# Performance work log

Measured on AMD Instinct MI355X. Metric: run time of the kernel, lower is better.

## Reference

```python
import jax, jax.numpy as jnp
import numpy as np

BINS = 10
LOSS_WEIGHT = 1.0
N = 8388608


def setup_inputs() -> dict:
    key = jax.random.key(0)
    k1, k2 = jax.random.split(key)
    pred = jax.random.normal(k1, (N, 2), dtype=jnp.float32)
    target = jax.random.randint(k2, (N,), 0, 2, dtype=jnp.int64)
    return {"pred": pred, "target": target}


def reference(pred, target):
    # one-hot binary target, as in torch scatter_(1, target, 1) with class_num=2
    tgt = jax.nn.one_hot(target, 2, dtype=pred.dtype)  # [N, 2]
    # label_weight defaults to ones -> all elements valid
    tot = jnp.maximum(jnp.asarray(pred.size, pred.dtype), 1.0)

    # gradient magnitude g = |sigmoid(pred).detach() - target|, in [0, 1]
    g = jnp.abs(jax.nn.sigmoid(jax.lax.stop_gradient(pred)) - tgt)

    # edges are i/bins with edges[-1] += 1e-6, so bin = min(floor(g*bins), bins-1)
    bin_idx = jnp.clip((g * BINS).astype(jnp.int32), 0, BINS - 1)  # [N, 2]

    # histogram of valid samples per bin (all valid here)
    counts = jax.ops.segment_sum(
        jnp.ones((pred.size,), pred.dtype), bin_idx.reshape(-1), num_segments=BINS
    )  # [BINS]

    n_nonempty = (counts > 0).sum()
    per_bin_w = jnp.where(counts > 0, tot / jnp.maximum(counts, 1.0), 0.0)  # [BINS]
    weights = per_bin_w[bin_idx]  # [N, 2]
    weights = jnp.where(
        n_nonempty > 0, weights / n_nonempty.astype(pred.dtype), weights
    )
    weights = jax.lax.stop_gradient(weights)

    # stable BCE with logits: max(x,0) - x*t + log(1 + exp(-|x|))
    bce = jnp.maximum(pred, 0.0) - pred * tgt + jnp.log1p(jnp.exp(-jnp.abs(pred)))
    loss = jnp.sum(weights * bce) / tot
    return loss * LOSS_WEIGHT
```

## Files before the change

### kernel.cpp

```cpp
#include <hip/hip_runtime.h>

#define BINS 10
#define BLOCK 256
#define GRID 2048
#define NCOPY 8
#define CSTRIDE 32

#define LOG2E 1.44269504088896340736f
#define LN2   0.6931471805599453094


__constant__ const float THR[9] = {
    -2.1972246f, -1.3862944f, -0.84729785f, -0.40546511f, 0.0f,
     0.40546511f, 0.84729785f, 1.3862944f,  2.1972246f };

__global__ void ghmc_init(double* ws) {
    int i = threadIdx.x;
    if (i < NCOPY * CSTRIDE) ws[i] = 0.0;
}

__device__ __forceinline__ void proc(float y, float* __restrict__ s,
                                     unsigned* __restrict__ c) {
    y = fminf(fmaxf(y, -80.0f), 80.0f);
    float u  = __builtin_amdgcn_exp2f(y * LOG2E);
    float d  = 1.0f + u;
    float lg = __builtin_amdgcn_logf(d);
    s[0] += lg;
#pragma unroll
    for (int k = 0; k < 9; ++k) {
        bool cond = y >= THR[k];
        c[k] += (unsigned)__popcll(__ballot(cond));
        s[k + 1] += cond ? lg : 0.0f;
    }
}

__device__ __forceinline__ void proc_row(float x0, float x1, int t,
                                         float* __restrict__ s,
                                         unsigned* __restrict__ c) {
    unsigned s0 = (unsigned)(t ^ 1) << 31;
    unsigned s1 = s0 ^ 0x80000000u;
    proc(__uint_as_float(__float_as_uint(x0) ^ s0), s, c);
    proc(__uint_as_float(__float_as_uint(x1) ^ s1), s, c);
}

__global__ __launch_bounds__(BLOCK, 8) void ghmc_main(
    const float4* __restrict__ pred4,
    const int4*   __restrict__ tgt4,
    double* __restrict__ wsd,
    int nQuads, int nRows)
{
    const int tid = threadIdx.x;
    float    s[BINS];
    unsigned c[9];
#pragma unroll
    for (int b = 0; b < BINS; ++b) s[b] = 0.0f;
#pragma unroll
    for (int k = 0; k < 9; ++k) c[k] = 0u;

    for (int i = blockIdx.x * BLOCK + tid; i < nQuads; i += GRID * BLOCK) {
        float4 pa = pred4[2 * i + 0];
        float4 pb = pred4[2 * i + 1];
        int4   tq = tgt4[i];
        proc_row(pa.x, pa.y, tq.x, s, c);
        proc_row(pa.z, pa.w, tq.y, s, c);
        proc_row(pb.x, pb.y, tq.z, s, c);
        proc_row(pb.z, pb.w, tq.w, s, c);
    }

    if (blockIdx.x == 0 && tid == 0) {
        const float* pf = (const float*)pred4;
        const int*   tf = (const int*)tgt4;
        for (int r = nQuads * 4; r < nRows; ++r)
            proc_row(pf[2 * r], pf[2 * r + 1], tf[r], s, c);
    }

#pragma unroll
    for (int off = 32; off > 0; off >>= 1) {
#pragma unroll
        for (int b = 0; b < BINS; ++b) s[b] += __shfl_down(s[b], off, 64);
    }

    __shared__ float    sred[4][BINS];
    __shared__ unsigned cred[4][9];
    const int wid  = tid >> 6;
    const int lane = tid & 63;
    if (lane == 0) {
#pragma unroll
        for (int b = 0; b < BINS; ++b) sred[wid][b] = s[b];
#pragma unroll
        for (int k = 0; k < 9; ++k) cred[wid][k] = c[k];
    }
    __syncthreads();

    double* wcopy = wsd + (blockIdx.x & (NCOPY - 1)) * CSTRIDE;
    if (tid < BINS) {
        float S = sred[0][tid] + sred[1][tid] + sred[2][tid] + sred[3][tid];
        atomicAdd(&wcopy[tid], (double)S);
    } else if (tid >= 16 && tid < 25) {
        int k = tid - 16;
        unsigned C = cred[0][k] + cred[1][k] + cred[2][k] + cred[3][k];
        atomicAdd(&wcopy[10 + k], (double)C);
    }
}

__global__ __launch_bounds__(64) void ghmc_fin(
    const double* __restrict__ wsd, float* __restrict__ out, int nRows)
{
    const int tid = threadIdx.x;
    __shared__ double vals[19];
    if (tid < 19) {
        double a = 0.0;
#pragma unroll
        for (int r = 0; r < NCOPY; ++r) a += wsd[r * CSTRIDE + tid];
        vals[tid] = a;
    }
    __syncthreads();
    if (tid == 0) {
        double C[BINS + 1], S[BINS + 1];
        C[0] = 2.0 * (double)nRows;
#pragma unroll
        for (int k = 1; k <= 9; ++k) C[k] = vals[9 + k];
        C[BINS] = 0.0;
#pragma unroll
        for (int b = 0; b < BINS; ++b) S[b] = vals[b];
        S[BINS] = 0.0;
        int nz = 0;
        double acc = 0.0;
#pragma unroll
        for (int b = 0; b < BINS; ++b) {
            double cnt = C[b] - C[b + 1];
            double sm  = (S[b] - S[b + 1]) * LN2;
            if (cnt > 0.0) { nz++; acc += sm / cnt; }
        }
        out[0] = (float)((nz > 0) ? (acc / (double)nz) : 0.0);
    }
}

extern "C" void kernel_launch(void* const* d_in, const int* in_sizes, int n_in,
                              void* d_out, int out_size, void* d_ws, size_t ws_size,
                              hipStream_t stream) {
    const float* pred = (const float*)d_in[0];
    const int* target = (const int*)d_in[1];
    const int nRows = in_sizes[1];
    const int nQuads = nRows / 4;
    double* wsd = (double*)d_ws;
    float* out = (float*)d_out;

    ghmc_init<<<1, 256, 0, stream>>>(wsd);
    ghmc_main<<<GRID, BLOCK, 0, stream>>>(
        (const float4*)pred, (const int4*)target, wsd, nQuads, nRows);
    ghmc_fin<<<1, 64, 0, stream>>>(wsd, out, nRows);
}
```

Before: 33.34 us.

## Replace threshold ballot scan with per-thread LDS histogram of bin counts and sums

Each element now gets its bin index directly from the sigmoid value and increments a private per-thread float2 (count, log-sum) slot in shared memory. This replaces the nine threshold compares, ballots, popcounts and conditional adds per element. The loop is also restructured so each wave reads contiguous float4/int2 chunks, and the block reduction runs over the LDS histogram before the atomics. It adds a reciprocal and a read-modify-write to shared memory per element, and per-thread float counts could lose precision.

New measurement: 34.43 us. 1.03x slower.

```diff
diff --git a/kernel.cpp b/kernel.cpp
--- a/kernel.cpp
+++ b/kernel.cpp
@@ -10,105 +10,120 @@
 #define LN2   0.6931471805599453094
 
 
-__constant__ const float THR[9] = {
-    -2.1972246f, -1.3862944f, -0.84729785f, -0.40546511f, 0.0f,
-     0.40546511f, 0.84729785f, 1.3862944f,  2.1972246f };
-
 __global__ void ghmc_init(double* ws) {
     int i = threadIdx.x;
     if (i < NCOPY * CSTRIDE) ws[i] = 0.0;
 }
 
-__device__ __forceinline__ void proc(float y, float* __restrict__ s,
-                                     unsigned* __restrict__ c) {
+__device__ __forceinline__ void proc(float y, float2* __restrict__ hcol) {
     y = fminf(fmaxf(y, -80.0f), 80.0f);
     float u  = __builtin_amdgcn_exp2f(y * LOG2E);
     float d  = 1.0f + u;
+    float r  = __builtin_amdgcn_rcpf(d);
     float lg = __builtin_amdgcn_logf(d);
-    s[0] += lg;
-#pragma unroll
-    for (int k = 0; k < 9; ++k) {
-        bool cond = y >= THR[k];
-        c[k] += (unsigned)__popcll(__ballot(cond));
-        s[k + 1] += cond ? lg : 0.0f;
-    }
+    float sg = u * r;
+    int b = (int)(sg * 10.0f);
+    b = b > (BINS - 1) ? (BINS - 1) : b;
+    float2* h = hcol + (b << 8);
+    float2 v = *h;
+    v.x += 1.0f;
+    v.y += lg;
+    *h = v;
 }
 
 __device__ __forceinline__ void proc_row(float x0, float x1, int t,
-                                         float* __restrict__ s,
-                                         unsigned* __restrict__ c) {
+                                         float2* __restrict__ hcol) {
     unsigned s0 = (unsigned)(t ^ 1) << 31;
     unsigned s1 = s0 ^ 0x80000000u;
-    proc(__uint_as_float(__float_as_uint(x0) ^ s0), s, c);
-    proc(__uint_as_float(__float_as_uint(x1) ^ s1), s, c);
+    proc(__uint_as_float(__float_as_uint(x0) ^ s0), hcol);
+    proc(__uint_as_float(__float_as_uint(x1) ^ s1), hcol);
 }
 
 __global__ __launch_bounds__(BLOCK, 8) void ghmc_main(
     const float4* __restrict__ pred4,
-    const int4*   __restrict__ tgt4,
+    const int2*   __restrict__ tgt2,
     double* __restrict__ wsd,
-    int nQuads, int nRows)
+    int nF4, int nRows)
 {
+    __shared__ float2 hist[BINS][BLOCK];
     const int tid = threadIdx.x;
-    float    s[BINS];
-    unsigned c[9];
 #pragma unroll
-    for (int b = 0; b < BINS; ++b) s[b] = 0.0f;
+    for (int b = 0; b < BINS; ++b) hist[b][tid] = make_float2(0.f, 0.f);
+
+    float2* hcol = &hist[0][tid];
+
+    const int lane = tid & 63;
+    const int gw   = (blockIdx.x * BLOCK + tid) >> 6;
+    const int NW   = (GRID * BLOCK) >> 6;
+
+    for (int w = gw; w * 256 < nF4; w += NW) {
+        int base = w * 256 + lane;
 #pragma unroll
-    for (int k = 0; k < 9; ++k) c[k] = 0u;
-
-    for (int i = blockIdx.x * BLOCK + tid; i < nQuads; i += GRID * BLOCK) {
-        float4 pa = pred4[2 * i + 0];
-        float4 pb = pred4[2 * i + 1];
-        int4   tq = tgt4[i];
-        proc_row(pa.x, pa.y, tq.x, s, c);
-        proc_row(pa.z, pa.w, tq.y, s, c);
-        proc_row(pb.x, pb.y, tq.z, s, c);
-        proc_row(pb.z, pb.w, tq.w, s, c);
+        for (int j = 0; j < 4; ++j) {
+            int idx = base + j * 64;
+            if (idx < nF4) {
+                float4 p = pred4[idx];
+                int2   t = tgt2[idx];
+                proc_row(p.x, p.y, t.x, hcol);
+                proc_row(p.z, p.w, t.y, hcol);
+            }
+        }
     }
 
-    if (blockIdx.x == 0 && tid == 0) {
+    if (blockIdx.x == 0 && tid == 0 && (nRows & 1)) {
         const float* pf = (const float*)pred4;
-        const int*   tf = (const int*)tgt4;
-        for (int r = nQuads * 4; r < nRows; ++r)
-            proc_row(pf[2 * r], pf[2 * r + 1], tf[r], s, c);
+        const int*   tf = (const int*)tgt2;
+        int r = nRows - 1;
+        proc_row(pf[2 * r], pf[2 * r + 1], tf[r], hcol);
     }
 
+    __syncthreads();
+
+    if (tid < 128) {
 #pragma unroll
-    for (int off = 32; off > 0; off >>= 1) {
+        for (int b = 0; b < BINS; ++b) {
+            float2 x = hist[b][tid], y = hist[b][tid + 128];
+            hist[b][tid] = make_float2(x.x + y.x, x.y + y.y);
+        }
+    }
+    __syncthreads();
+    __shared__ float svals[2 * BINS];
+    if (tid < 64) {
+        float cx[BINS], cy[BINS];
 #pragma unroll
-        for (int b = 0; b < BINS; ++b) s[b] += __shfl_down(s[b], off, 64);
-    }
-
-    __shared__ float    sred[4][BINS];
-    __shared__ unsigned cred[4][9];
-    const int wid  = tid >> 6;
-    const int lane = tid & 63;
-    if (lane == 0) {
+        for (int b = 0; b < BINS; ++b) {
+            float2 x = hist[b][tid], y = hist[b][tid + 64];
+            cx[b] = x.x + y.x;
+            cy[b] = x.y + y.y;
+        }
 #pragma unroll
-        for (int b = 0; b < BINS; ++b) sred[wid][b] = s[b];
+        for (int off = 32; off > 0; off >>= 1) {
 #pragma unroll
-        for (int k = 0; k < 9; ++k) cred[wid][k] = c[k];
+            for (int b = 0; b < BINS; ++b) {
+                cx[b] += __shfl_down(cx[b], off, 64);
+                cy[b] += __shfl_down(cy[b], off, 64);
+            }
+        }
+        if (tid == 0) {
+#pragma unroll
+            for (int b = 0; b < BINS; ++b) {
+                svals[b]        = cx[b];
+                svals[BINS + b] = cy[b];
+            }
+        }
     }
     __syncthreads();
 
     double* wcopy = wsd + (blockIdx.x & (NCOPY - 1)) * CSTRIDE;
-    if (tid < BINS) {
-        float S = sred[0][tid] + sred[1][tid] + sred[2][tid] + sred[3][tid];
-        atomicAdd(&wcopy[tid], (double)S);
-    } else if (tid >= 16 && tid < 25) {
-        int k = tid - 16;
-        unsigned C = cred[0][k] + cred[1][k] + cred[2][k] + cred[3][k];
-        atomicAdd(&wcopy[10 + k], (double)C);
-    }
+    if (tid < 2 * BINS) atomicAdd(&wcopy[tid], (double)svals[tid]);
 }
 
 __global__ __launch_bounds__(64) void ghmc_fin(
-    const double* __restrict__ wsd, float* __restrict__ out, int nRows)
+    const double* __restrict__ wsd, float* __restrict__ out)
 {
     const int tid = threadIdx.x;
-    __shared__ double vals[19];
-    if (tid < 19) {
+    __shared__ double vals[2 * BINS];
+    if (tid < 2 * BINS) {
         double a = 0.0;
 #pragma unroll
         for (int r = 0; r < NCOPY; ++r) a += wsd[r * CSTRIDE + tid];
@@ -116,20 +131,12 @@
     }
     __syncthreads();
     if (tid == 0) {
-        double C[BINS + 1], S[BINS + 1];
-        C[0] = 2.0 * (double)nRows;
-#pragma unroll
-        for (int k = 1; k <= 9; ++k) C[k] = vals[9 + k];
-        C[BINS] = 0.0;
-#pragma unroll
-        for (int b = 0; b < BINS; ++b) S[b] = vals[b];
-        S[BINS] = 0.0;
         int nz = 0;
         double acc = 0.0;
 #pragma unroll
         for (int b = 0; b < BINS; ++b) {
-            double cnt = C[b] - C[b + 1];
-            double sm  = (S[b] - S[b + 1]) * LN2;
+            double cnt = vals[b];
+            double sm  = vals[BINS + b] * LN2;
             if (cnt > 0.0) { nz++; acc += sm / cnt; }
         }
         out[0] = (float)((nz > 0) ? (acc / (double)nz) : 0.0);
@@ -142,12 +149,12 @@
     const float* pred = (const float*)d_in[0];
     const int* target = (const int*)d_in[1];
     const int nRows = in_sizes[1];
-    const int nQuads = nRows / 4;
+    const int nF4 = nRows / 2;
     double* wsd = (double*)d_ws;
     float* out = (float*)d_out;
 
     ghmc_init<<<1, 256, 0, stream>>>(wsd);
     ghmc_main<<<GRID, BLOCK, 0, stream>>>(
-        (const float4*)pred, (const int4*)target, wsd, nQuads, nRows);
-    ghmc_fin<<<1, 64, 0, stream>>>(wsd, out, nRows);
+        (const float4*)pred, (const int2*)target, wsd, nF4, nRows);
+    ghmc_fin<<<1, 64, 0, stream>>>(wsd, out);
 }
```
